# Kernel tuning notes

Measured on AMD Instinct MI355X. Metric: run time of the kernel, lower is better.

The kernel has to match this reference:

```python
import jax, jax.numpy as jnp
import numpy as np

INPUT_SIZE = 16
HIDDEN = 256


def setup_inputs() -> dict:
    key = jax.random.key(0)
    ks = jax.random.split(key, 12)
    B, T, F, H = 512, 168, INPUT_SIZE, HIDDEN
    s_ih = 1.0 / np.sqrt(H)
    def u(k, shape):
        return jax.random.uniform(k, shape, jnp.float32, -s_ih, s_ih)
    return {
        "x": jax.random.normal(ks[0], (B, T, F), jnp.float32),
        # LSTM params, torch gate order (i, f, g, o) stacked along dim 0
        "w_ih": u(ks[1], (4 * H, F)),
        "w_hh": u(ks[2], (4 * H, H)),
        "b_ih": u(ks[3], (4 * H,)),
        "b_hh": u(ks[4], (4 * H,)),
        # MLP params
        "fc1_w": u(ks[5], (128, H)),
        "fc1_b": u(ks[6], (128,)),
        "fc2_w": u(ks[7], (64, 128)),
        "fc2_b": u(ks[8], (64,)),
        "fc3_w": u(ks[9], (1, 64)),
        "fc3_b": u(ks[10], (1,)),
    }


def _lstm(x, w_ih, w_hh, b_ih, b_hh):
    B, T, F = x.shape
    H = w_hh.shape[1]
    # Precompute input contribution for all timesteps: [B, T, 4H]
    x_proj = jnp.einsum("btf,gf->btg", x, w_ih) + b_ih + b_hh

    def step(carry, xp_t):
        h, c = carry
        gates = xp_t + h @ w_hh.T  # [B, 4H]
        i, f, g, o = jnp.split(gates, 4, axis=-1)
        i = jax.nn.sigmoid(i)
        f = jax.nn.sigmoid(f)
        g = jnp.tanh(g)
        o = jax.nn.sigmoid(o)
        c = f * c + i * g
        h = o * jnp.tanh(c)
        return (h, c), h

    h0 = jnp.zeros((B, H), x.dtype)
    c0 = jnp.zeros((B, H), x.dtype)
    (_, _), hs = jax.lax.scan(step, (h0, c0), jnp.swapaxes(x_proj, 0, 1))
    return jnp.swapaxes(hs, 0, 1)  # [B, T, H]


def reference(x, w_ih, w_hh, b_ih, b_hh, fc1_w, fc1_b, fc2_w, fc2_b, fc3_w, fc3_b):
    h = _lstm(x, w_ih, w_hh, b_ih, b_hh)          # [B, T, H]
    h = jax.nn.relu(h @ fc1_w.T + fc1_b)           # [B, T, 128]
    h = jax.nn.relu(h @ fc2_w.T + fc2_b)           # [B, T, 64]
    out = h @ fc3_w.T + fc3_b                      # [B, T, 1]
    return out
```

## Files before the change

kernel.cpp:

```cpp
#include <hip/hip_runtime.h>

typedef _Float16 half8 __attribute__((ext_vector_type(8)));
typedef float floatx4 __attribute__((ext_vector_type(4)));

#define Bsz 512
#define Tsz 168
#define Fsz 16
#define Hsz 256
#define KTILES 9
#define LDS_K 296

#define WSW_OFF   0
#define BIAS_OFF  589824
#define FC1_OFF   593920
#define FC2_OFF   659456
#define HH_OFF    675840
#define XBUF_OFF  (HH_OFF + 44040192)

__global__ void k_swz_whh(const float* __restrict__ w_hh,
                          const float* __restrict__ w_ih,
                          _Float16* __restrict__ wsw) {
    int tile = blockIdx.x;
    int nt = tile / KTILES, kt = tile - nt * KTILES;
    int lane = threadIdx.x;
    int n_in = lane & 15, kg = lane >> 4;
    int J = nt >> 2, g = nt & 3;
    int n_orig = g * 256 + J * 16 + n_in;
    half8 v;
#pragma unroll
    for (int e = 0; e < 8; ++e) {
        int k = kt * 32 + kg * 8 + e;
        float f;
        if (k < 256)      f = w_hh[n_orig * 256 + k];
        else if (k < 272) f = w_ih[n_orig * 16 + (k - 256)];
        else              f = 0.0f;
        v[e] = (_Float16)f;
    }
    ((half8*)wsw)[tile * 64 + lane] = v;
}

__global__ void k_bias(const float* __restrict__ b_ih,
                       const float* __restrict__ b_hh,
                       float* __restrict__ bias) {
    int id = blockIdx.x * 256 + threadIdx.x;
    int nt = id >> 4, n = id & 15;
    int J = nt >> 2, g = nt & 3;
    int n_orig = g * 256 + J * 16 + n;
    bias[id] = b_ih[n_orig] + b_hh[n_orig];
}

__global__ void k_swz_fc(const float* __restrict__ w, _Float16* __restrict__ dst,
                         int ktiles, int K) {
    int tile = blockIdx.x;
    int nt = tile / ktiles, kt = tile - nt * ktiles;
    int lane = threadIdx.x;
    int n_in = lane & 15, kg = lane >> 4;
    int n_orig = nt * 16 + n_in;
    half8 v;
#pragma unroll
    for (int e = 0; e < 8; ++e) {
        int k = kt * 32 + kg * 8 + e;
        v[e] = (_Float16)w[n_orig * K + k];
    }
    ((half8*)dst)[tile * 64 + lane] = v;
}

__global__ __launch_bounds__(512, 1) void k_lstm10(
    const float* __restrict__ x, const _Float16* __restrict__ wsw,
    const float* __restrict__ bias, unsigned* __restrict__ hh32,
    unsigned long long* __restrict__ xbuf) {
    __shared__ __align__(16) _Float16 wsh[16 * 8 * 512];
    __shared__ __align__(16) _Float16 h_lds[16][LDS_K];
    __shared__ float glds[4][16][68];

    const int tid = threadIdx.x;
    const int wave = tid >> 6, lane = tid & 63;
    const int n_in = lane & 15, quad = lane >> 4;
    const int bb = blockIdx.x >> 2, ng = blockIdx.x & 3;
    const int b0 = bb * 16;
    const int Jl = wave & 3;
    const int gp = wave >> 2;

    {
        const float4* srcw = (const float4*)wsw;
        float4* dstw = (float4*)wsh;
#pragma unroll
        for (int it = 0; it < 16; ++it) {
            int i = it * 512 + tid;
            dstw[i] = srcw[(size_t)(ng * 16 + (i >> 9)) * 576 + (i & 511)];
        }
    }
    float bs[2];
    half8 wx[2];
#pragma unroll
    for (int gg = 0; gg < 2; ++gg) {
        const int nt = ng * 16 + Jl * 4 + gp * 2 + gg;
        bs[gg] = bias[nt * 16 + n_in];
        wx[gg] = ((const half8*)wsw)[((size_t)nt * KTILES + 8) * 64 + lane];
    }

    for (int i = tid; i < 16 * LDS_K; i += 512)
        ((_Float16*)h_lds)[i] = (_Float16)0.0f;
    __syncthreads();
    if (tid < 256) {
        int m = tid >> 4, f = tid & 15;
        h_lds[m][Hsz + f] = (_Float16)x[((b0 + m) * Tsz + 0) * Fsz + f];
    }
    __syncthreads();

    const int cm = tid >> 5, cj = tid & 31;
    float c_st[2] = {0.f, 0.f};

    for (int t = 0; t < Tsz; ++t) {
        half8 afr[KTILES];
#pragma unroll
        for (int kt = 0; kt < KTILES; ++kt)
            afr[kt] = *(const half8*)&h_lds[n_in][kt * 32 + quad * 8];

        floatx4 acc[2] = {(floatx4){0.f,0.f,0.f,0.f}, (floatx4){0.f,0.f,0.f,0.f}};
#pragma unroll
        for (int gg = 0; gg < 2; ++gg) {
            const int nt_l = Jl * 4 + gp * 2 + gg;
#pragma unroll
            for (int kt = 0; kt < 8; ++kt) {
                half8 bfr = *(const half8*)&wsh[((nt_l << 3) + kt) * 512 + lane * 8];
                acc[gg] = __builtin_amdgcn_mfma_f32_16x16x32_f16(afr[kt], bfr, acc[gg], 0, 0, 0);
            }
            acc[gg] = __builtin_amdgcn_mfma_f32_16x16x32_f16(afr[8], wx[gg], acc[gg], 0, 0, 0);
        }

#pragma unroll
        for (int gg = 0; gg < 2; ++gg)
#pragma unroll
            for (int r = 0; r < 4; ++r)
                glds[gp * 2 + gg][quad * 4 + r][Jl * 16 + n_in] = acc[gg][r] + bs[gg];
        __syncthreads();

        union { _Float16 f[2]; unsigned u; } pk;
#pragma unroll
        for (int e = 0; e < 2; ++e) {
            int jl = 2 * cj + e;
            float ig = glds[0][cm][jl];
            float fg = glds[1][cm][jl];
            float gg_ = glds[2][cm][jl];
            float og = glds[3][cm][jl];
            float si = 1.0f / (1.0f + __expf(-ig));
            float sf = 1.0f / (1.0f + __expf(-fg));
            float tg = 1.0f - 2.0f / (__expf(2.0f * gg_) + 1.0f);
            float so = 1.0f / (1.0f + __expf(-og));
            float c = sf * c_st[e] + si * tg;
            c_st[e] = c;
            float th = 1.0f - 2.0f / (__expf(2.0f * c) + 1.0f);
            pk.f[e] = (_Float16)(so * th);
        }
        *(unsigned*)&h_lds[cm][ng * 64 + 2 * cj] = pk.u;
        hh32[((size_t)(b0 + cm) * Tsz + t) * 128 + ng * 32 + cj] = pk.u;

        const size_t rb = ((size_t)((bb * 2 + (t & 1)) * 16));
        if (t + 1 < Tsz) {
            unsigned long long pv = ((unsigned long long)pk.u << 32) | (unsigned)(t + 1);
            __hip_atomic_store(&xbuf[(rb + cm) * 128 + ng * 32 + cj], pv,
                               __ATOMIC_RELAXED, __HIP_MEMORY_SCOPE_AGENT);

            float xr = 0.0f;
            if (tid < 256)
                xr = x[((b0 + (tid >> 4)) * Tsz + (t + 1)) * Fsz + (tid & 15)];

            const unsigned want = (unsigned)(t + 1);
            unsigned long long* p1 = &xbuf[(rb + cm) * 128 + ((ng + 1) & 3) * 32 + cj];
            unsigned long long* p2 = &xbuf[(rb + cm) * 128 + ((ng + 2) & 3) * 32 + cj];
            unsigned long long* p3 = &xbuf[(rb + cm) * 128 + ((ng + 3) & 3) * 32 + cj];
            unsigned long long v1 = __hip_atomic_load(p1, __ATOMIC_RELAXED,
                                                      __HIP_MEMORY_SCOPE_AGENT);
            unsigned long long v2 = __hip_atomic_load(p2, __ATOMIC_RELAXED,
                                                      __HIP_MEMORY_SCOPE_AGENT);
            unsigned long long v3 = __hip_atomic_load(p3, __ATOMIC_RELAXED,
                                                      __HIP_MEMORY_SCOPE_AGENT);
            while ((unsigned)v1 != want || (unsigned)v2 != want || (unsigned)v3 != want) {
                if ((unsigned)v1 != want)
                    v1 = __hip_atomic_load(p1, __ATOMIC_RELAXED, __HIP_MEMORY_SCOPE_AGENT);
                if ((unsigned)v2 != want)
                    v2 = __hip_atomic_load(p2, __ATOMIC_RELAXED, __HIP_MEMORY_SCOPE_AGENT);
                if ((unsigned)v3 != want)
                    v3 = __hip_atomic_load(p3, __ATOMIC_RELAXED, __HIP_MEMORY_SCOPE_AGENT);
            }
            *(unsigned*)&h_lds[cm][((ng + 1) & 3) * 64 + 2 * cj] = (unsigned)(v1 >> 32);
            *(unsigned*)&h_lds[cm][((ng + 2) & 3) * 64 + 2 * cj] = (unsigned)(v2 >> 32);
            *(unsigned*)&h_lds[cm][((ng + 3) & 3) * 64 + 2 * cj] = (unsigned)(v3 >> 32);
            if (tid < 256)
                h_lds[tid >> 4][Hsz + (tid & 15)] = (_Float16)xr;
            __syncthreads();
        }
    }
}

__global__ __launch_bounds__(256) void k_mlp(
    const _Float16* __restrict__ hh, const _Float16* __restrict__ w1f,
    const _Float16* __restrict__ w2f, const float* __restrict__ b1,
    const float* __restrict__ b2, const float* __restrict__ w3,
    const float* __restrict__ b3, float* __restrict__ out) {
    __shared__ _Float16 st1[4][16][136];
    __shared__ _Float16 st2[4][16][72];

    const int tid = threadIdx.x;
    const int wave = tid >> 6, lane = tid & 63;
    const int n_in = lane & 15, quad = lane >> 4;
    const int tok0 = blockIdx.x * 64 + wave * 16;

    half8 afr[8];
#pragma unroll
    for (int kt = 0; kt < 8; ++kt)
        afr[kt] = *(const half8*)&hh[(size_t)(tok0 + n_in) * 256 + kt * 32 + quad * 8];
    const half8* w1 = (const half8*)w1f;
#pragma unroll
    for (int nt = 0; nt < 8; ++nt) {
        floatx4 a = (floatx4){0.f, 0.f, 0.f, 0.f};
#pragma unroll
        for (int kt = 0; kt < 8; ++kt)
            a = __builtin_amdgcn_mfma_f32_16x16x32_f16(afr[kt], w1[(nt * 8 + kt) * 64 + lane], a, 0, 0, 0);
        float bb = b1[nt * 16 + n_in];
#pragma unroll
        for (int r = 0; r < 4; ++r) {
            float v = a[r] + bb;
            st1[wave][quad * 4 + r][nt * 16 + n_in] = (_Float16)(v > 0.f ? v : 0.f);
        }
    }
    __syncthreads();

    half8 a2[4];
#pragma unroll
    for (int kt = 0; kt < 4; ++kt)
        a2[kt] = *(const half8*)&st1[wave][n_in][kt * 32 + quad * 8];
    const half8* w2 = (const half8*)w2f;
#pragma unroll
    for (int nt = 0; nt < 4; ++nt) {
        floatx4 a = (floatx4){0.f, 0.f, 0.f, 0.f};
#pragma unroll
        for (int kt = 0; kt < 4; ++kt)
            a = __builtin_amdgcn_mfma_f32_16x16x32_f16(a2[kt], w2[(nt * 4 + kt) * 64 + lane], a, 0, 0, 0);
        float bb = b2[nt * 16 + n_in];
#pragma unroll
        for (int r = 0; r < 4; ++r) {
            float v = a[r] + bb;
            st2[wave][quad * 4 + r][nt * 16 + n_in] = (_Float16)(v > 0.f ? v : 0.f);
        }
    }
    __syncthreads();

    float p = 0.0f;
#pragma unroll
    for (int e = 0; e < 16; ++e)
        p += (float)st2[wave][n_in][quad * 16 + e] * w3[quad * 16 + e];
    p += __shfl_down(p, 32);
    p += __shfl_down(p, 16);
    if (quad == 0) out[tok0 + n_in] = p + b3[0];
}

extern "C" void kernel_launch(void* const* d_in, const int* in_sizes, int n_in,
                              void* d_out, int out_size, void* d_ws, size_t ws_size,
                              hipStream_t stream) {
    const float* x     = (const float*)d_in[0];
    const float* w_ih  = (const float*)d_in[1];
    const float* w_hh  = (const float*)d_in[2];
    const float* b_ih  = (const float*)d_in[3];
    const float* b_hh  = (const float*)d_in[4];
    const float* fc1_w = (const float*)d_in[5];
    const float* fc1_b = (const float*)d_in[6];
    const float* fc2_w = (const float*)d_in[7];
    const float* fc2_b = (const float*)d_in[8];
    const float* fc3_w = (const float*)d_in[9];
    const float* fc3_b = (const float*)d_in[10];

    char* ws = (char*)d_ws;
    _Float16* wsw  = (_Float16*)(ws + WSW_OFF);
    float*    bias = (float*)(ws + BIAS_OFF);
    _Float16* w1f  = (_Float16*)(ws + FC1_OFF);
    _Float16* w2f  = (_Float16*)(ws + FC2_OFF);
    _Float16* hhist= (_Float16*)(ws + HH_OFF);
    unsigned long long* xbuf = (unsigned long long*)(ws + XBUF_OFF);

    k_swz_whh<<<576, 64, 0, stream>>>(w_hh, w_ih, wsw);
    k_bias<<<4, 256, 0, stream>>>(b_ih, b_hh, bias);
    k_swz_fc<<<64, 64, 0, stream>>>(fc1_w, w1f, 8, 256);
    k_swz_fc<<<16, 64, 0, stream>>>(fc2_w, w2f, 4, 128);
    k_lstm10<<<128, 512, 0, stream>>>(x, wsw, bias, (unsigned*)hhist, xbuf);
    k_mlp<<<Bsz * Tsz / 64, 256, 0, stream>>>(hhist, w1f, w2f, fc1_b, fc2_b,
                                              fc3_w, fc3_b, (float*)d_out);
}
```

Measured before the change: 507.6 us.

## Merge prep kernels, remap LSTM block indices, persistent MLP with LDS weights

Folds the four weight/bias preparation kernels into a single launch, which cuts launch overhead. It also changes how LSTM block indices map to (batch tile, gate group), so the four cooperating blocks of a batch tile now land on differently spaced CUs. The MLP becomes a persistent 224-block kernel that stages the fc1/fc2 fragments in LDS once and loops over token chunks, instead of reading them from global memory in every one of 1344 blocks. The index remap may change the latency of the cross-block flag exchange, and the persistent MLP has lower occupancy.

Measured after the change: 467.8 us. -7.8%, faster.

```diff
diff --git a/kernel.cpp b/kernel.cpp
--- a/kernel.cpp
+++ b/kernel.cpp
@@ -17,55 +17,59 @@
 #define HH_OFF    675840
 #define XBUF_OFF  (HH_OFF + 44040192)
 
-__global__ void k_swz_whh(const float* __restrict__ w_hh,
-                          const float* __restrict__ w_ih,
-                          _Float16* __restrict__ wsw) {
-    int tile = blockIdx.x;
-    int nt = tile / KTILES, kt = tile - nt * KTILES;
-    int lane = threadIdx.x;
-    int n_in = lane & 15, kg = lane >> 4;
-    int J = nt >> 2, g = nt & 3;
-    int n_orig = g * 256 + J * 16 + n_in;
-    half8 v;
-#pragma unroll
-    for (int e = 0; e < 8; ++e) {
-        int k = kt * 32 + kg * 8 + e;
-        float f;
-        if (k < 256)      f = w_hh[n_orig * 256 + k];
-        else if (k < 272) f = w_ih[n_orig * 16 + (k - 256)];
-        else              f = 0.0f;
-        v[e] = (_Float16)f;
-    }
-    ((half8*)wsw)[tile * 64 + lane] = v;
+__global__ __launch_bounds__(256) void k_prep(
+    const float* __restrict__ w_hh, const float* __restrict__ w_ih,
+    const float* __restrict__ b_ih, const float* __restrict__ b_hh,
+    const float* __restrict__ fc1_w, const float* __restrict__ fc2_w,
+    _Float16* __restrict__ wsw, float* __restrict__ bias,
+    _Float16* __restrict__ w1f, _Float16* __restrict__ w2f) {
+    const int b = blockIdx.x, tid = threadIdx.x;
+    const int lane = tid & 63, sub = tid >> 6;
+    if (b < 144) {
+        int tile = b * 4 + sub;
+        int nt = tile / KTILES, kt = tile - nt * KTILES;
+        int n_in = lane & 15, kg = lane >> 4;
+        int J = nt >> 2, g = nt & 3;
+        int n_orig = g * 256 + J * 16 + n_in;
+        half8 v;
+#pragma unroll
+        for (int e = 0; e < 8; ++e) {
+            int k = kt * 32 + kg * 8 + e;
+            float f;
+            if (k < 256)      f = w_hh[n_orig * 256 + k];
+            else if (k < 272) f = w_ih[n_orig * 16 + (k - 256)];
+            else              f = 0.0f;
+            v[e] = (_Float16)f;
+        }
+        ((half8*)wsw)[tile * 64 + lane] = v;
+    } else if (b < 148) {
+        int id = (b - 144) * 256 + tid;
+        int nt = id >> 4, n = id & 15;
+        int J = nt >> 2, g = nt & 3;
+        int n_orig = g * 256 + J * 16 + n;
+        bias[id] = b_ih[n_orig] + b_hh[n_orig];
+    } else if (b < 164) {
+        int tile = (b - 148) * 4 + sub;
+        int nt = tile >> 3, kt = tile & 7;
+        int n_in = lane & 15, kg = lane >> 4;
+        half8 v;
+#pragma unroll
+        for (int e = 0; e < 8; ++e)
+            v[e] = (_Float16)fc1_w[(nt * 16 + n_in) * 256 + kt * 32 + kg * 8 + e];
+        ((half8*)w1f)[tile * 64 + lane] = v;
+    } else {
+        int tile = (b - 164) * 4 + sub;
+        int nt = tile >> 2, kt = tile & 3;
+        int n_in = lane & 15, kg = lane >> 4;
+        half8 v;
+#pragma unroll
+        for (int e = 0; e < 8; ++e)
+            v[e] = (_Float16)fc2_w[(nt * 16 + n_in) * 128 + kt * 32 + kg * 8 + e];
+        ((half8*)w2f)[tile * 64 + lane] = v;
+    }
 }
 
-__global__ void k_bias(const float* __restrict__ b_ih,
-                       const float* __restrict__ b_hh,
-                       float* __restrict__ bias) {
-    int id = blockIdx.x * 256 + threadIdx.x;
-    int nt = id >> 4, n = id & 15;
-    int J = nt >> 2, g = nt & 3;
-    int n_orig = g * 256 + J * 16 + n;
-    bias[id] = b_ih[n_orig] + b_hh[n_orig];
-}
-
-__global__ void k_swz_fc(const float* __restrict__ w, _Float16* __restrict__ dst,
-                         int ktiles, int K) {
-    int tile = blockIdx.x;
-    int nt = tile / ktiles, kt = tile - nt * ktiles;
-    int lane = threadIdx.x;
-    int n_in = lane & 15, kg = lane >> 4;
-    int n_orig = nt * 16 + n_in;
-    half8 v;
-#pragma unroll
-    for (int e = 0; e < 8; ++e) {
-        int k = kt * 32 + kg * 8 + e;
-        v[e] = (_Float16)w[n_orig * K + k];
-    }
-    ((half8*)dst)[tile * 64 + lane] = v;
-}
-
-__global__ __launch_bounds__(512, 1) void k_lstm10(
+__global__ __launch_bounds__(512, 1) void k_lstm12(
     const float* __restrict__ x, const _Float16* __restrict__ wsw,
     const float* __restrict__ bias, unsigned* __restrict__ hh32,
     unsigned long long* __restrict__ xbuf) {
@@ -76,7 +80,7 @@
     const int tid = threadIdx.x;
     const int wave = tid >> 6, lane = tid & 63;
     const int n_in = lane & 15, quad = lane >> 4;
-    const int bb = blockIdx.x >> 2, ng = blockIdx.x & 3;
+    const int bb = blockIdx.x & 31, ng = blockIdx.x >> 5;
     const int b0 = bb * 16;
     const int Jl = wave & 3;
     const int gp = wave >> 2;
@@ -194,66 +198,83 @@
     }
 }
 
-__global__ __launch_bounds__(256) void k_mlp(
+__global__ __launch_bounds__(512, 1) void k_mlp3(
     const _Float16* __restrict__ hh, const _Float16* __restrict__ w1f,
     const _Float16* __restrict__ w2f, const float* __restrict__ b1,
     const float* __restrict__ b2, const float* __restrict__ w3,
     const float* __restrict__ b3, float* __restrict__ out) {
-    __shared__ _Float16 st1[4][16][136];
-    __shared__ _Float16 st2[4][16][72];
+    __shared__ __align__(16) _Float16 w1sh[64 * 512];
+    __shared__ __align__(16) _Float16 w2sh[16 * 512];
+    __shared__ _Float16 st1[8][16][136];
+    __shared__ _Float16 st2[8][16][72];
 
     const int tid = threadIdx.x;
     const int wave = tid >> 6, lane = tid & 63;
     const int n_in = lane & 15, quad = lane >> 4;
-    const int tok0 = blockIdx.x * 64 + wave * 16;
-
-    half8 afr[8];
-#pragma unroll
-    for (int kt = 0; kt < 8; ++kt)
-        afr[kt] = *(const half8*)&hh[(size_t)(tok0 + n_in) * 256 + kt * 32 + quad * 8];
-    const half8* w1 = (const half8*)w1f;
-#pragma unroll
-    for (int nt = 0; nt < 8; ++nt) {
-        floatx4 a = (floatx4){0.f, 0.f, 0.f, 0.f};
+
+    {
+        float4* d1 = (float4*)w1sh;
+        const float4* s1 = (const float4*)w1f;
+#pragma unroll
+        for (int it = 0; it < 8; ++it) d1[it * 512 + tid] = s1[it * 512 + tid];
+        float4* d2 = (float4*)w2sh;
+        const float4* s2 = (const float4*)w2f;
+#pragma unroll
+        for (int it = 0; it < 2; ++it) d2[it * 512 + tid] = s2[it * 512 + tid];
+    }
+    __syncthreads();
+
+    for (int chunk = blockIdx.x; chunk < (Bsz * Tsz) / 128; chunk += gridDim.x) {
+        const int tok0 = chunk * 128 + wave * 16;
+
+        half8 afr[8];
 #pragma unroll
         for (int kt = 0; kt < 8; ++kt)
-            a = __builtin_amdgcn_mfma_f32_16x16x32_f16(afr[kt], w1[(nt * 8 + kt) * 64 + lane], a, 0, 0, 0);
-        float bb = b1[nt * 16 + n_in];
-#pragma unroll
-        for (int r = 0; r < 4; ++r) {
-            float v = a[r] + bb;
-            st1[wave][quad * 4 + r][nt * 16 + n_in] = (_Float16)(v > 0.f ? v : 0.f);
-        }
-    }
-    __syncthreads();
-
-    half8 a2[4];
-#pragma unroll
-    for (int kt = 0; kt < 4; ++kt)
-        a2[kt] = *(const half8*)&st1[wave][n_in][kt * 32 + quad * 8];
-    const half8* w2 = (const half8*)w2f;
-#pragma unroll
-    for (int nt = 0; nt < 4; ++nt) {
-        floatx4 a = (floatx4){0.f, 0.f, 0.f, 0.f};
+            afr[kt] = *(const half8*)&hh[(size_t)(tok0 + n_in) * 256 + kt * 32 + quad * 8];
+#pragma unroll
+        for (int nt = 0; nt < 8; ++nt) {
+            floatx4 a = (floatx4){0.f, 0.f, 0.f, 0.f};
+#pragma unroll
+            for (int kt = 0; kt < 8; ++kt) {
+                half8 bfr = *(const half8*)&w1sh[(nt * 8 + kt) * 512 + lane * 8];
+                a = __builtin_amdgcn_mfma_f32_16x16x32_f16(afr[kt], bfr, a, 0, 0, 0);
+            }
+            float bb = b1[nt * 16 + n_in];
+#pragma unroll
+            for (int r = 0; r < 4; ++r) {
+                float v = a[r] + bb;
+                st1[wave][quad * 4 + r][nt * 16 + n_in] = (_Float16)(v > 0.f ? v : 0.f);
+            }
+        }
+
+        half8 a2[4];
 #pragma unroll
         for (int kt = 0; kt < 4; ++kt)
-            a = __builtin_amdgcn_mfma_f32_16x16x32_f16(a2[kt], w2[(nt * 4 + kt) * 64 + lane], a, 0, 0, 0);
-        float bb = b2[nt * 16 + n_in];
-#pragma unroll
-        for (int r = 0; r < 4; ++r) {
-            float v = a[r] + bb;
-            st2[wave][quad * 4 + r][nt * 16 + n_in] = (_Float16)(v > 0.f ? v : 0.f);
-        }
-    }
-    __syncthreads();
-
-    float p = 0.0f;
-#pragma unroll
-    for (int e = 0; e < 16; ++e)
-        p += (float)st2[wave][n_in][quad * 16 + e] * w3[quad * 16 + e];
-    p += __shfl_down(p, 32);
-    p += __shfl_down(p, 16);
-    if (quad == 0) out[tok0 + n_in] = p + b3[0];
+            a2[kt] = *(const half8*)&st1[wave][n_in][kt * 32 + quad * 8];
+#pragma unroll
+        for (int nt = 0; nt < 4; ++nt) {
+            floatx4 a = (floatx4){0.f, 0.f, 0.f, 0.f};
+#pragma unroll
+            for (int kt = 0; kt < 4; ++kt) {
+                half8 bfr = *(const half8*)&w2sh[(nt * 4 + kt) * 512 + lane * 8];
+                a = __builtin_amdgcn_mfma_f32_16x16x32_f16(a2[kt], bfr, a, 0, 0, 0);
+            }
+            float bb = b2[nt * 16 + n_in];
+#pragma unroll
+            for (int r = 0; r < 4; ++r) {
+                float v = a[r] + bb;
+                st2[wave][quad * 4 + r][nt * 16 + n_in] = (_Float16)(v > 0.f ? v : 0.f);
+            }
+        }
+
+        float p = 0.0f;
+#pragma unroll
+        for (int e = 0; e < 16; ++e)
+            p += (float)st2[wave][n_in][quad * 16 + e] * w3[quad * 16 + e];
+        p += __shfl_down(p, 32);
+        p += __shfl_down(p, 16);
+        if (quad == 0) out[tok0 + n_in] = p + b3[0];
+    }
 }
 
 extern "C" void kernel_launch(void* const* d_in, const int* in_sizes, int n_in,
@@ -279,11 +300,9 @@
     _Float16* hhist= (_Float16*)(ws + HH_OFF);
     unsigned long long* xbuf = (unsigned long long*)(ws + XBUF_OFF);
 
-    k_swz_whh<<<576, 64, 0, stream>>>(w_hh, w_ih, wsw);
-    k_bias<<<4, 256, 0, stream>>>(b_ih, b_hh, bias);
-    k_swz_fc<<<64, 64, 0, stream>>>(fc1_w, w1f, 8, 256);
-    k_swz_fc<<<16, 64, 0, stream>>>(fc2_w, w2f, 4, 128);
-    k_lstm10<<<128, 512, 0, stream>>>(x, wsw, bias, (unsigned*)hhist, xbuf);
-    k_mlp<<<Bsz * Tsz / 64, 256, 0, stream>>>(hhist, w1f, w2f, fc1_b, fc2_b,
-                                              fc3_w, fc3_b, (float*)d_out);
+    k_prep<<<168, 256, 0, stream>>>(w_hh, w_ih, b_ih, b_hh, fc1_w, fc2_w,
+                                    wsw, bias, w1f, w2f);
+    k_lstm12<<<128, 512, 0, stream>>>(x, wsw, bias, (unsigned*)hhist, xbuf);
+    k_mlp3<<<224, 512, 0, stream>>>(hhist, w1f, w2f, fc1_b, fc2_b,
+                                    fc3_w, fc3_b, (float*)d_out);
 }
```
